# Kernel optimization log

Measured on AMD Instinct MI355X. Metric: run time of the kernel, lower is better.

Reference implementation:

```python
import jax, jax.numpy as jnp
import numpy as np

N_NODES = 50000
N_EDGES = 500000
IN_CH = 128
OUT_CH = 256


def setup_inputs() -> dict:
    key = jax.random.key(0)
    k1, k2, k3, k4, k5 = jax.random.split(key, 5)
    x = jax.random.normal(k1, (N_NODES, IN_CH), dtype=jnp.float32)
    edge_index = jax.random.randint(k2, (2, N_EDGES), 0, N_NODES, dtype=jnp.int64)
    edge_weight = jax.random.normal(k3, (N_EDGES,), dtype=jnp.float32)
    # GCNConv linear weight (xavier-uniform) and bias (zeros in torch init; use randn for generality)
    limit = float(np.sqrt(6.0 / (IN_CH + OUT_CH)))
    W = jax.random.uniform(k4, (IN_CH, OUT_CH), minval=-limit, maxval=limit, dtype=jnp.float32)
    b = jnp.zeros((OUT_CH,), dtype=jnp.float32)
    return {"x": x, "W": W, "b": b, "edge_index": edge_index, "edge_weight": edge_weight}


def reference(x, W, b, edge_index, edge_weight):
    N = x.shape[0]
    # GCN wrapper applies sigmoid to edge weights before GCNConv
    ew = jax.nn.sigmoid(edge_weight)
    # gcn_norm: add self-loops with weight 1
    loop = jnp.arange(N, dtype=edge_index.dtype)
    row = jnp.concatenate([edge_index[0], loop])  # source nodes
    col = jnp.concatenate([edge_index[1], loop])  # target nodes
    w = jnp.concatenate([ew, jnp.ones((N,), dtype=x.dtype)])
    # degree on target index, symmetric normalization
    deg = jax.ops.segment_sum(w, col, num_segments=N)
    dinv = jnp.where(deg > 0, jax.lax.rsqrt(deg), jnp.zeros_like(deg))
    norm = dinv[row] * w * dinv[col]  # [E+N]
    # linear transform first (GCNConv: lin has no bias; bias added after aggregation)
    h = x @ W  # [N, OUT_CH]
    msg = h[row] * norm[:, None]  # gather + scale  [E+N, OUT_CH]
    out = jax.ops.segment_sum(msg, col, num_segments=N) + b
    return out
```

## Files before the change

### kernel.cpp

```cpp
#include <hip/hip_runtime.h>
#include <hip/hip_bf16.h>
#include <hip/hip_fp16.h>
#include <math.h>

#define NN 50000
#define NE 500000
#define IC 128
#define OC 256
#define NPAD 50176
#define NB 196
#define NEB 1954
#define CAP 64

typedef short bf16x8 __attribute__((ext_vector_type(8)));
typedef float f32x4 __attribute__((ext_vector_type(4)));

static __device__ inline unsigned short f2b(float f) {
    __hip_bfloat16 h = __float2bfloat16(f);
    return *reinterpret_cast<unsigned short*>(&h);
}
static __device__ inline float b2f(short u) {
    unsigned v = ((unsigned)(unsigned short)u) << 16;
    return __int_as_float(v);
}
static __device__ inline float h2f(unsigned short h) {
    __half v = __ushort_as_half(h);
    return __half2float(v);
}

__global__ void k_init(unsigned long long* __restrict__ deg64) {
    int i = blockIdx.x * 256 + threadIdx.x;
    deg64[i] = (unsigned long long)(1u << 24);
}

__global__ void k_pass1(const int* __restrict__ row,
                        const int* __restrict__ col,
                        const float* __restrict__ ew,
                        unsigned long long* __restrict__ deg64,
                        unsigned* __restrict__ epack,
                        const float* __restrict__ x,
                        unsigned short* __restrict__ xb,
                        const float* __restrict__ W,
                        unsigned short* __restrict__ WT) {
    int g = blockIdx.x * 256 + threadIdx.x;
    if (g < NE) {
        int c = col[g];
        float w = 1.0f / (1.0f + expf(-ew[g]));
        unsigned long long pack = (1ull << 32) | (unsigned long long)(unsigned)(w * 16777216.0f);
        unsigned long long old = atomicAdd(&deg64[c], pack);
        int ord = (int)(old >> 32);
        if (ord < CAP) {
            unsigned short wh = __half_as_ushort(__float2half_rn(w));
            unsigned p = ((unsigned)wh << 16) | (unsigned)row[g];
            epack[(size_t)c * CAP + ord] = p;
        }
    }
    const int NX = NN * (IC / 4);
    for (int i = g; i < NX; i += NEB * 256) {
        float4 v = ((const float4*)x)[i];
        ushort4 o;
        o.x = f2b(v.x); o.y = f2b(v.y); o.z = f2b(v.z); o.w = f2b(v.w);
        ((ushort4*)xb)[i] = o;
    }
    if (g < IC * OC) {
        int k = g >> 8;
        int n = g & 255;
        WT[n * IC + k] = f2b(W[g]);
    }
}

__global__ void k_dinv(const unsigned long long* __restrict__ deg64,
                       float* __restrict__ dinv) {
    int i = blockIdx.x * 256 + threadIdx.x;
    unsigned long long v = deg64[i];
    float deg = (float)(unsigned)v * (1.0f / 16777216.0f);
    dinv[i] = rsqrtf(deg);
}

__global__ __launch_bounds__(256) void k_gather_gemm(
        const unsigned short* __restrict__ xb,
        const unsigned long long* __restrict__ deg64,
        const unsigned* __restrict__ epack,
        const float* __restrict__ dinv,
        const unsigned short* __restrict__ WT,
        const float* __restrict__ bias,
        float* __restrict__ out) {
    __shared__ __align__(16) unsigned short a[32][136];

    const int base = blockIdx.x * 32;
    const int g = threadIdx.x >> 3;
    const int l8 = threadIdx.x & 7;
    const int n = base + g;
    const bf16x8* xv = (const bf16x8*)xb;

    float acc[16];
    if (n < NN) {
        float di = dinv[n];
        unsigned long long dv = deg64[n];
        int cnt = (int)(dv >> 32);
        if (cnt > CAP) cnt = CAP;
        float s2 = di * di;

        bf16x8 xs0 = xv[(size_t)n * 16 + l8];
        bf16x8 xs1 = xv[(size_t)n * 16 + 8 + l8];
        #pragma unroll
        for (int c = 0; c < 8; ++c) { acc[c] = b2f(xs0[c]) * s2; acc[8 + c] = b2f(xs1[c]) * s2; }

        const unsigned* ep = epack + (size_t)n * CAP;
        int e = 0;
        uint2 pq = *(const uint2*)ep;
        for (; e + 2 <= cnt; e += 2) {
            unsigned p0 = pq.x, p1 = pq.y;
            pq = *(const uint2*)(ep + e + 2);
            int r0 = (int)(p0 & 0xFFFFu);
            int r1 = (int)(p1 & 0xFFFFu);
            float w0 = h2f((unsigned short)(p0 >> 16)) * dinv[r0] * di;
            float w1 = h2f((unsigned short)(p1 >> 16)) * dinv[r1] * di;
            bf16x8 v00 = xv[(size_t)r0 * 16 + l8];
            bf16x8 v01 = xv[(size_t)r0 * 16 + 8 + l8];
            bf16x8 v10 = xv[(size_t)r1 * 16 + l8];
            bf16x8 v11 = xv[(size_t)r1 * 16 + 8 + l8];
            #pragma unroll
            for (int c = 0; c < 8; ++c) { acc[c] += b2f(v00[c]) * w0; acc[8 + c] += b2f(v01[c]) * w0; }
            #pragma unroll
            for (int c = 0; c < 8; ++c) { acc[c] += b2f(v10[c]) * w1; acc[8 + c] += b2f(v11[c]) * w1; }
        }
        if (e < cnt) {
            unsigned p = pq.x;
            int r = (int)(p & 0xFFFFu);
            float w = h2f((unsigned short)(p >> 16)) * dinv[r] * di;
            bf16x8 v0 = xv[(size_t)r * 16 + l8];
            bf16x8 v1 = xv[(size_t)r * 16 + 8 + l8];
            #pragma unroll
            for (int c = 0; c < 8; ++c) { acc[c] += b2f(v0[c]) * w; acc[8 + c] += b2f(v1[c]) * w; }
        }
    } else {
        #pragma unroll
        for (int c = 0; c < 16; ++c) acc[c] = 0.0f;
    }

    bf16x8 o0, o1;
    #pragma unroll
    for (int c = 0; c < 8; ++c) { o0[c] = (short)f2b(acc[c]); o1[c] = (short)f2b(acc[8 + c]); }
    *(bf16x8*)(&a[g][l8 * 8]) = o0;
    *(bf16x8*)(&a[g][64 + l8 * 8]) = o1;

    __syncthreads();

    const int w = threadIdx.x >> 6;
    const int lane = threadIdx.x & 63;
    const int n0 = w * 64;
    const int lm = lane & 15;
    const int lk = (lane >> 4) * 8;

    f32x4 acc4[2][4] = {};
    #pragma unroll
    for (int ks = 0; ks < 4; ++ks) {
        const int k0 = ks * 32 + lk;
        bf16x8 wf[4], af[2];
        #pragma unroll
        for (int j = 0; j < 4; ++j)
            wf[j] = *(const bf16x8*)(WT + (size_t)(n0 + j * 16 + lm) * IC + k0);
        #pragma unroll
        for (int i = 0; i < 2; ++i)
            af[i] = *(const bf16x8*)(&a[i * 16 + lm][k0]);
        #pragma unroll
        for (int i = 0; i < 2; ++i)
            #pragma unroll
            for (int j = 0; j < 4; ++j)
                acc4[i][j] = __builtin_amdgcn_mfma_f32_16x16x32_bf16(wf[j], af[i], acc4[i][j], 0, 0, 0);
    }

    const int mcol = lane & 15;
    const int nb4 = (lane >> 4) * 4;
    #pragma unroll
    for (int i = 0; i < 2; ++i) {
        int m = base + i * 16 + mcol;
        if (m < NN) {
            #pragma unroll
            for (int j = 0; j < 4; ++j) {
                int nn = n0 + j * 16 + nb4;
                float4 bv = *(const float4*)&bias[nn];
                float4 ov;
                ov.x = acc4[i][j][0] + bv.x;
                ov.y = acc4[i][j][1] + bv.y;
                ov.z = acc4[i][j][2] + bv.z;
                ov.w = acc4[i][j][3] + bv.w;
                *(float4*)(out + (size_t)m * OC + nn) = ov;
            }
        }
    }
}

extern "C" void kernel_launch(void* const* d_in, const int* in_sizes, int n_in,
                              void* d_out, int out_size, void* d_ws, size_t ws_size,
                              hipStream_t stream) {
    const float* x  = (const float*)d_in[0];
    const float* W  = (const float*)d_in[1];
    const float* b  = (const float*)d_in[2];
    const int*   ei = (const int*)d_in[3];
    const float* ew = (const float*)d_in[4];
    const int* row = ei;
    const int* col = ei + NE;
    float* out = (float*)d_out;

    char* w0 = (char*)d_ws;
    unsigned long long* deg64 = (unsigned long long*)w0;  w0 += NPAD * 8;
    float* dinv  = (float*)w0;                   w0 += NPAD * 4;
    unsigned* epack = (unsigned*)w0;             w0 += ((size_t)NPAD * CAP + 64) * 4;
    unsigned short* WT   = (unsigned short*)w0;  w0 += IC * OC * 2;
    unsigned short* xb   = (unsigned short*)w0;

    k_init       <<<NB, 256, 0, stream>>>(deg64);
    k_pass1      <<<NEB, 256, 0, stream>>>(row, col, ew, deg64, epack, x, xb, W, WT);
    k_dinv       <<<NB, 256, 0, stream>>>(deg64, dinv);
    k_gather_gemm<<<(NN + 31) / 32, 256, 0, stream>>>(xb, deg64, epack, dinv, WT, b, out);
}
```

Measured before the change: 168.8 us.

## Split each node's edge gather across two half-groups and shrink tile to 16 nodes

The gather-GEMM kernel now processes 16 nodes per block instead of 32. Each node's edge list is split between two 8-lane halves, which are combined with a shuffle-xor reduction, so twice as many threads gather per node. The idea is to shorten the per-thread serial gather chain and raise memory-level parallelism and occupancy (launch_bounds 256,8). In exchange, each block does less MFMA work per W-tile load, so W is re-read from cache twice as often, and the prefetch of edge-list entries is dropped.

Result: slower. 174.4 us (+3.3%).

```diff
diff --git a/kernel.cpp b/kernel.cpp
--- a/kernel.cpp
+++ b/kernel.cpp
@@ -77,7 +77,7 @@
     dinv[i] = rsqrtf(deg);
 }
 
-__global__ __launch_bounds__(256) void k_gather_gemm(
+__global__ __launch_bounds__(256, 8) void k_gather_gemm(
         const unsigned short* __restrict__ xb,
         const unsigned long long* __restrict__ deg64,
         const unsigned* __restrict__ epack,
@@ -85,65 +85,72 @@
         const unsigned short* __restrict__ WT,
         const float* __restrict__ bias,
         float* __restrict__ out) {
-    __shared__ __align__(16) unsigned short a[32][136];
-
-    const int base = blockIdx.x * 32;
-    const int g = threadIdx.x >> 3;
-    const int l8 = threadIdx.x & 7;
+    __shared__ __align__(16) unsigned short a[16][136];
+
+    const int base = blockIdx.x * 16;
+    const int g = threadIdx.x >> 4;
+    const int sub = threadIdx.x & 15;
+    const int l8 = sub & 7;
+    const int h = sub >> 3;
     const int n = base + g;
     const bf16x8* xv = (const bf16x8*)xb;
 
+    float di = dinv[n];
+    unsigned long long dv = deg64[n];
+    int cnt = (int)(dv >> 32);
+    if (cnt > CAP) cnt = CAP;
+    int mid = (cnt + 1) >> 1;
+    int lo = h ? mid : 0;
+    int hi = h ? cnt : mid;
+
+    float selfw = h ? 0.0f : di * di;
+    bf16x8 xs0 = xv[(size_t)n * 16 + l8];
+    bf16x8 xs1 = xv[(size_t)n * 16 + 8 + l8];
     float acc[16];
-    if (n < NN) {
-        float di = dinv[n];
-        unsigned long long dv = deg64[n];
-        int cnt = (int)(dv >> 32);
-        if (cnt > CAP) cnt = CAP;
-        float s2 = di * di;
-
-        bf16x8 xs0 = xv[(size_t)n * 16 + l8];
-        bf16x8 xs1 = xv[(size_t)n * 16 + 8 + l8];
-        #pragma unroll
-        for (int c = 0; c < 8; ++c) { acc[c] = b2f(xs0[c]) * s2; acc[8 + c] = b2f(xs1[c]) * s2; }
-
-        const unsigned* ep = epack + (size_t)n * CAP;
-        int e = 0;
-        uint2 pq = *(const uint2*)ep;
-        for (; e + 2 <= cnt; e += 2) {
-            unsigned p0 = pq.x, p1 = pq.y;
-            pq = *(const uint2*)(ep + e + 2);
-            int r0 = (int)(p0 & 0xFFFFu);
-            int r1 = (int)(p1 & 0xFFFFu);
-            float w0 = h2f((unsigned short)(p0 >> 16)) * dinv[r0] * di;
-            float w1 = h2f((unsigned short)(p1 >> 16)) * dinv[r1] * di;
-            bf16x8 v00 = xv[(size_t)r0 * 16 + l8];
-            bf16x8 v01 = xv[(size_t)r0 * 16 + 8 + l8];
-            bf16x8 v10 = xv[(size_t)r1 * 16 + l8];
-            bf16x8 v11 = xv[(size_t)r1 * 16 + 8 + l8];
-            #pragma unroll
-            for (int c = 0; c < 8; ++c) { acc[c] += b2f(v00[c]) * w0; acc[8 + c] += b2f(v01[c]) * w0; }
-            #pragma unroll
-            for (int c = 0; c < 8; ++c) { acc[c] += b2f(v10[c]) * w1; acc[8 + c] += b2f(v11[c]) * w1; }
-        }
-        if (e < cnt) {
-            unsigned p = pq.x;
-            int r = (int)(p & 0xFFFFu);
-            float w = h2f((unsigned short)(p >> 16)) * dinv[r] * di;
-            bf16x8 v0 = xv[(size_t)r * 16 + l8];
-            bf16x8 v1 = xv[(size_t)r * 16 + 8 + l8];
-            #pragma unroll
-            for (int c = 0; c < 8; ++c) { acc[c] += b2f(v0[c]) * w; acc[8 + c] += b2f(v1[c]) * w; }
-        }
+    #pragma unroll
+    for (int c = 0; c < 8; ++c) { acc[c] = b2f(xs0[c]) * selfw; acc[8 + c] = b2f(xs1[c]) * selfw; }
+
+    const unsigned* ep = epack + (size_t)n * CAP;
+    int e = lo;
+    for (; e + 2 <= hi; e += 2) {
+        unsigned p0 = ep[e];
+        unsigned p1 = ep[e + 1];
+        int r0 = (int)(p0 & 0xFFFFu);
+        int r1 = (int)(p1 & 0xFFFFu);
+        float w0 = h2f((unsigned short)(p0 >> 16)) * dinv[r0] * di;
+        float w1 = h2f((unsigned short)(p1 >> 16)) * dinv[r1] * di;
+        bf16x8 v00 = xv[(size_t)r0 * 16 + l8];
+        bf16x8 v01 = xv[(size_t)r0 * 16 + 8 + l8];
+        bf16x8 v10 = xv[(size_t)r1 * 16 + l8];
+        bf16x8 v11 = xv[(size_t)r1 * 16 + 8 + l8];
+        #pragma unroll
+        for (int c = 0; c < 8; ++c) { acc[c] += b2f(v00[c]) * w0; acc[8 + c] += b2f(v01[c]) * w0; }
+        #pragma unroll
+        for (int c = 0; c < 8; ++c) { acc[c] += b2f(v10[c]) * w1; acc[8 + c] += b2f(v11[c]) * w1; }
+    }
+    if (e < hi) {
+        unsigned p = ep[e];
+        int r = (int)(p & 0xFFFFu);
+        float w = h2f((unsigned short)(p >> 16)) * dinv[r] * di;
+        bf16x8 v0 = xv[(size_t)r * 16 + l8];
+        bf16x8 v1 = xv[(size_t)r * 16 + 8 + l8];
+        #pragma unroll
+        for (int c = 0; c < 8; ++c) { acc[c] += b2f(v0[c]) * w; acc[8 + c] += b2f(v1[c]) * w; }
+    }
+
+    #pragma unroll
+    for (int c = 0; c < 16; ++c) acc[c] += __shfl_xor(acc[c], 8);
+
+    bf16x8 o;
+    if (h == 0) {
+        #pragma unroll
+        for (int c = 0; c < 8; ++c) o[c] = (short)f2b(acc[c]);
+        *(bf16x8*)(&a[g][l8 * 8]) = o;
     } else {
         #pragma unroll
-        for (int c = 0; c < 16; ++c) acc[c] = 0.0f;
-    }
-
-    bf16x8 o0, o1;
-    #pragma unroll
-    for (int c = 0; c < 8; ++c) { o0[c] = (short)f2b(acc[c]); o1[c] = (short)f2b(acc[8 + c]); }
-    *(bf16x8*)(&a[g][l8 * 8]) = o0;
-    *(bf16x8*)(&a[g][64 + l8 * 8]) = o1;
+        for (int c = 0; c < 8; ++c) o[c] = (short)f2b(acc[8 + c]);
+        *(bf16x8*)(&a[g][64 + l8 * 8]) = o;
+    }
 
     __syncthreads();
 
@@ -153,42 +160,33 @@
     const int lm = lane & 15;
     const int lk = (lane >> 4) * 8;
 
-    f32x4 acc4[2][4] = {};
+    f32x4 acc4[4] = {};
     #pragma unroll
     for (int ks = 0; ks < 4; ++ks) {
         const int k0 = ks * 32 + lk;
-        bf16x8 wf[4], af[2];
+        bf16x8 wf[4];
         #pragma unroll
         for (int j = 0; j < 4; ++j)
             wf[j] = *(const bf16x8*)(WT + (size_t)(n0 + j * 16 + lm) * IC + k0);
-        #pragma unroll
-        for (int i = 0; i < 2; ++i)
-            af[i] = *(const bf16x8*)(&a[i * 16 + lm][k0]);
-        #pragma unroll
-        for (int i = 0; i < 2; ++i)
-            #pragma unroll
-            for (int j = 0; j < 4; ++j)
-                acc4[i][j] = __builtin_amdgcn_mfma_f32_16x16x32_bf16(wf[j], af[i], acc4[i][j], 0, 0, 0);
+        bf16x8 af = *(const bf16x8*)(&a[lm][k0]);
+        #pragma unroll
+        for (int j = 0; j < 4; ++j)
+            acc4[j] = __builtin_amdgcn_mfma_f32_16x16x32_bf16(wf[j], af, acc4[j], 0, 0, 0);
     }
 
     const int mcol = lane & 15;
     const int nb4 = (lane >> 4) * 4;
-    #pragma unroll
-    for (int i = 0; i < 2; ++i) {
-        int m = base + i * 16 + mcol;
-        if (m < NN) {
-            #pragma unroll
-            for (int j = 0; j < 4; ++j) {
-                int nn = n0 + j * 16 + nb4;
-                float4 bv = *(const float4*)&bias[nn];
-                float4 ov;
-                ov.x = acc4[i][j][0] + bv.x;
-                ov.y = acc4[i][j][1] + bv.y;
-                ov.z = acc4[i][j][2] + bv.z;
-                ov.w = acc4[i][j][3] + bv.w;
-                *(float4*)(out + (size_t)m * OC + nn) = ov;
-            }
-        }
+    const int m = base + mcol;
+    #pragma unroll
+    for (int j = 0; j < 4; ++j) {
+        int nn = n0 + j * 16 + nb4;
+        float4 bv = *(const float4*)&bias[nn];
+        float4 ov;
+        ov.x = acc4[j][0] + bv.x;
+        ov.y = acc4[j][1] + bv.y;
+        ov.z = acc4[j][2] + bv.z;
+        ov.w = acc4[j][3] + bv.w;
+        *(float4*)(out + (size_t)m * OC + nn) = ov;
     }
 }
 
@@ -214,5 +212,5 @@
     k_init       <<<NB, 256, 0, stream>>>(deg64);
     k_pass1      <<<NEB, 256, 0, stream>>>(row, col, ew, deg64, epack, x, xb, W, WT);
     k_dinv       <<<NB, 256, 0, stream>>>(deg64, dinv);
-    k_gather_gemm<<<(NN + 31) / 32, 256, 0, stream>>>(xb, deg64, epack, dinv, WT, b, out);
-}
+    k_gather_gemm<<<NN / 16, 256, 0, stream>>>(xb, deg64, epack, dinv, WT, b, out);
+}
```

## Prescale x by dinv during bf16 conversion and unroll gather by four

Applied to the files above, without the earlier changes.

Moves the x-to-bf16 conversion out of the edge pass into a new per-node kernel that also computes dinv and stores x already multiplied by dinv[row]. The gather then no longer does a dependent random dinv[r] load per edge, and the self term needs only a single di factor. The edge loop now processes four neighbors per iteration with uint4 epack loads, which increases memory-level parallelism and register use. Pre-scaling in bf16 changes rounding slightly.

New measurement: 162.2 us. -3.9%, faster.

```diff
diff --git a/kernel.cpp b/kernel.cpp
--- a/kernel.cpp
+++ b/kernel.cpp
@@ -38,8 +38,6 @@
                         const float* __restrict__ ew,
                         unsigned long long* __restrict__ deg64,
                         unsigned* __restrict__ epack,
-                        const float* __restrict__ x,
-                        unsigned short* __restrict__ xb,
                         const float* __restrict__ W,
                         unsigned short* __restrict__ WT) {
     int g = blockIdx.x * 256 + threadIdx.x;
@@ -55,13 +53,6 @@
             epack[(size_t)c * CAP + ord] = p;
         }
     }
-    const int NX = NN * (IC / 4);
-    for (int i = g; i < NX; i += NEB * 256) {
-        float4 v = ((const float4*)x)[i];
-        ushort4 o;
-        o.x = f2b(v.x); o.y = f2b(v.y); o.z = f2b(v.z); o.w = f2b(v.w);
-        ((ushort4*)xb)[i] = o;
-    }
     if (g < IC * OC) {
         int k = g >> 8;
         int n = g & 255;
@@ -69,12 +60,26 @@
     }
 }
 
-__global__ void k_dinv(const unsigned long long* __restrict__ deg64,
-                       float* __restrict__ dinv) {
-    int i = blockIdx.x * 256 + threadIdx.x;
-    unsigned long long v = deg64[i];
+__global__ __launch_bounds__(256) void k_scale(
+        const unsigned long long* __restrict__ deg64,
+        const float* __restrict__ x,
+        unsigned short* __restrict__ xb,
+        float* __restrict__ dinv) {
+    int t = threadIdx.x;
+    int n = blockIdx.x * 16 + (t >> 4);
+    int l = t & 15;
+    unsigned long long v = deg64[n];
     float deg = (float)(unsigned)v * (1.0f / 16777216.0f);
-    dinv[i] = rsqrtf(deg);
+    float di = rsqrtf(deg);
+    if (l == 0) dinv[n] = di;
+    const float4* xr = (const float4*)(x + (size_t)n * IC + l * 8);
+    float4 a0 = xr[0], a1 = xr[1];
+    bf16x8 o;
+    o[0] = (short)f2b(a0.x * di); o[1] = (short)f2b(a0.y * di);
+    o[2] = (short)f2b(a0.z * di); o[3] = (short)f2b(a0.w * di);
+    o[4] = (short)f2b(a1.x * di); o[5] = (short)f2b(a1.y * di);
+    o[6] = (short)f2b(a1.z * di); o[7] = (short)f2b(a1.w * di);
+    ((bf16x8*)xb)[(size_t)n * 16 + l] = o;
 }
 
 __global__ __launch_bounds__(256) void k_gather_gemm(
@@ -99,36 +104,47 @@
         unsigned long long dv = deg64[n];
         int cnt = (int)(dv >> 32);
         if (cnt > CAP) cnt = CAP;
-        float s2 = di * di;
 
         bf16x8 xs0 = xv[(size_t)n * 16 + l8];
         bf16x8 xs1 = xv[(size_t)n * 16 + 8 + l8];
         #pragma unroll
-        for (int c = 0; c < 8; ++c) { acc[c] = b2f(xs0[c]) * s2; acc[8 + c] = b2f(xs1[c]) * s2; }
+        for (int c = 0; c < 8; ++c) { acc[c] = b2f(xs0[c]) * di; acc[8 + c] = b2f(xs1[c]) * di; }
 
         const unsigned* ep = epack + (size_t)n * CAP;
+        uint4 q = *(const uint4*)ep;
         int e = 0;
-        uint2 pq = *(const uint2*)ep;
-        for (; e + 2 <= cnt; e += 2) {
-            unsigned p0 = pq.x, p1 = pq.y;
-            pq = *(const uint2*)(ep + e + 2);
-            int r0 = (int)(p0 & 0xFFFFu);
-            int r1 = (int)(p1 & 0xFFFFu);
-            float w0 = h2f((unsigned short)(p0 >> 16)) * dinv[r0] * di;
-            float w1 = h2f((unsigned short)(p1 >> 16)) * dinv[r1] * di;
+        for (; e + 4 <= cnt; e += 4) {
+            uint4 cur = q;
+            q = *(const uint4*)(ep + e + 4);
+            int r0 = (int)(cur.x & 0xFFFFu);
+            int r1 = (int)(cur.y & 0xFFFFu);
+            int r2 = (int)(cur.z & 0xFFFFu);
+            int r3 = (int)(cur.w & 0xFFFFu);
+            float w0 = h2f((unsigned short)(cur.x >> 16)) * di;
+            float w1 = h2f((unsigned short)(cur.y >> 16)) * di;
+            float w2 = h2f((unsigned short)(cur.z >> 16)) * di;
+            float w3 = h2f((unsigned short)(cur.w >> 16)) * di;
             bf16x8 v00 = xv[(size_t)r0 * 16 + l8];
             bf16x8 v01 = xv[(size_t)r0 * 16 + 8 + l8];
             bf16x8 v10 = xv[(size_t)r1 * 16 + l8];
             bf16x8 v11 = xv[(size_t)r1 * 16 + 8 + l8];
+            bf16x8 v20 = xv[(size_t)r2 * 16 + l8];
+            bf16x8 v21 = xv[(size_t)r2 * 16 + 8 + l8];
+            bf16x8 v30 = xv[(size_t)r3 * 16 + l8];
+            bf16x8 v31 = xv[(size_t)r3 * 16 + 8 + l8];
             #pragma unroll
             for (int c = 0; c < 8; ++c) { acc[c] += b2f(v00[c]) * w0; acc[8 + c] += b2f(v01[c]) * w0; }
             #pragma unroll
             for (int c = 0; c < 8; ++c) { acc[c] += b2f(v10[c]) * w1; acc[8 + c] += b2f(v11[c]) * w1; }
-        }
-        if (e < cnt) {
-            unsigned p = pq.x;
+            #pragma unroll
+            for (int c = 0; c < 8; ++c) { acc[c] += b2f(v20[c]) * w2; acc[8 + c] += b2f(v21[c]) * w2; }
+            #pragma unroll
+            for (int c = 0; c < 8; ++c) { acc[c] += b2f(v30[c]) * w3; acc[8 + c] += b2f(v31[c]) * w3; }
+        }
+        for (; e < cnt; ++e) {
+            unsigned p = ep[e];
             int r = (int)(p & 0xFFFFu);
-            float w = h2f((unsigned short)(p >> 16)) * dinv[r] * di;
+            float w = h2f((unsigned short)(p >> 16)) * di;
             bf16x8 v0 = xv[(size_t)r * 16 + l8];
             bf16x8 v1 = xv[(size_t)r * 16 + 8 + l8];
             #pragma unroll
@@ -207,12 +223,12 @@
     char* w0 = (char*)d_ws;
     unsigned long long* deg64 = (unsigned long long*)w0;  w0 += NPAD * 8;
     float* dinv  = (float*)w0;                   w0 += NPAD * 4;
-    unsigned* epack = (unsigned*)w0;             w0 += ((size_t)NPAD * CAP + 64) * 4;
+    unsigned* epack = (unsigned*)w0;             w0 += ((size_t)NPAD * CAP + 128) * 4;
     unsigned short* WT   = (unsigned short*)w0;  w0 += IC * OC * 2;
     unsigned short* xb   = (unsigned short*)w0;
 
     k_init       <<<NB, 256, 0, stream>>>(deg64);
-    k_pass1      <<<NEB, 256, 0, stream>>>(row, col, ew, deg64, epack, x, xb, W, WT);
-    k_dinv       <<<NB, 256, 0, stream>>>(deg64, dinv);
+    k_pass1      <<<NEB, 256, 0, stream>>>(row, col, ew, deg64, epack, W, WT);
+    k_scale      <<<NN / 16, 256, 0, stream>>>(deg64, x, xb, dinv);
     k_gather_gemm<<<(NN + 31) / 32, 256, 0, stream>>>(xb, deg64, epack, dinv, WT, b, out);
 }
```
